# Kernel optimization log

Measured on AMD Instinct MI355X. Metric: run time of the kernel, lower is better.

## Reference

```python
import jax, jax.numpy as jnp
import numpy as np
from jax import lax

B, N, M = 4, 16384, 2048
C_IN = 64
RADII = (0.2, 0.4)
KS = (32, 64)
MLPS = ((64, 64, 128), (64, 96, 128))
EPS = 1e-5


def setup_inputs() -> dict:
    key = jax.random.key(0)
    ks = jax.random.split(key, 32)
    inp = {}
    inp["xyz"] = jax.random.uniform(ks[0], (B, 3, N), jnp.float32)
    inp["feature"] = jax.random.normal(ks[1], (B, C_IN, N), jnp.float32)
    ki = 2
    for s, chans in enumerate(MLPS):
        cin = C_IN + 3  # use_xyz concatenates relative xyz
        for l, cout in enumerate(chans):
            inp[f"w{s}{l}"] = jax.random.normal(ks[ki], (cout, cin), jnp.float32) * (1.0 / np.sqrt(cin)); ki += 1
            inp[f"g{s}{l}"] = jnp.ones((cout,), jnp.float32)
            inp[f"b{s}{l}"] = jnp.zeros((cout,), jnp.float32)
            cin = cout
    return inp


def _fps(points):
    """Farthest point sampling. points [N,3] -> [M] int32 indices (starts at 0)."""
    n = points.shape[0]
    def step(carry, _):
        dists, last = carry
        d = jnp.sum((points - points[last]) ** 2, axis=-1)
        dists = jnp.minimum(dists, d)
        nxt = jnp.argmax(dists).astype(jnp.int32)
        return (dists, nxt), nxt
    init = (jnp.full((n,), 1e10, jnp.float32), jnp.int32(0))
    _, rest = lax.scan(step, init, None, length=M - 1)
    return jnp.concatenate([jnp.zeros((1,), jnp.int32), rest])


def _ball_query(xyz, new_xyz, radius, k):
    """xyz [B,3,N], new_xyz [B,3,M] -> [B,M,k] int32. First-found semantics: empty
    slots are filled with the first valid index (pointnet2 ball_query behavior)."""
    xyz = lax.stop_gradient(xyz)
    new_xyz = lax.stop_gradient(new_xyz)
    n = xyz.shape[-1]
    sq_x = jnp.sum(xyz ** 2, axis=1)          # [B,N]
    sq_c = jnp.sum(new_xyz ** 2, axis=1)      # [B,M]
    d2 = sq_c[:, :, None] + sq_x[:, None, :] - 2.0 * jnp.einsum('bdm,bdn->bmn', new_xyz, xyz)
    scores = jnp.where(d2 < radius * radius, jnp.arange(n, dtype=jnp.int32), n)
    idx = -lax.top_k(-scores, k)[0]           # k smallest indices (in order)
    first = idx[..., :1]
    idx = jnp.where(idx >= n, first, idx)
    return jnp.where(idx >= n, 0, idx)


def _group(feat, idx):
    """feat [B,C,N], idx [B,M,K] -> [B,C,M,K]"""
    return jax.vmap(lambda f, i: f[:, i])(feat, idx)


def _forward(xyz, feature, params):
    idx = jax.vmap(_fps)(jnp.transpose(lax.stop_gradient(xyz), (0, 2, 1)))  # [B,M]
    new_xyz = jnp.take_along_axis(xyz, idx[:, None, :].astype(jnp.int32), axis=2)  # [B,3,M]
    feats = []
    for s in range(len(MLPS)):
        nidx = _ball_query(xyz, new_xyz, RADII[s], KS[s])        # [B,M,K]
        gxyz = _group(xyz, nidx) - new_xyz[..., None]            # [B,3,M,K]
        x = jnp.concatenate([gxyz, _group(feature, nidx)], axis=1)  # [B,3+C,M,K]
        for l in range(len(MLPS[s])):
            w = params[f"w{s}{l}"]; g = params[f"g{s}{l}"]; b = params[f"b{s}{l}"]
            x = jnp.einsum('oc,bcmk->bomk', w, x)                # 1x1 conv
            mu = jnp.mean(x, axis=(0, 2, 3), keepdims=True)      # train-mode BN
            var = jnp.mean((x - mu) ** 2, axis=(0, 2, 3), keepdims=True)
            x = (x - mu) * lax.rsqrt(var + EPS)
            x = x * g[None, :, None, None] + b[None, :, None, None]
            x = jax.nn.relu(x)
        feats.append(jnp.max(x, axis=3))                         # max over neighbors
    return new_xyz, jnp.concatenate(feats, axis=1)               # [B,3,M], [B,256,M]


def reference(xyz, feature, w00, g00, b00, w01, g01, b01, w02, g02, b02,
              w10, g10, b10, w11, g11, b11, w12, g12, b12):
    params = dict(w00=w00, g00=g00, b00=b00, w01=w01, g01=g01, b01=b01,
                  w02=w02, g02=g02, b02=b02, w10=w10, g10=g10, b10=b10,
                  w11=w11, g11=g11, b11=b11, w12=w12, g12=g12, b12=b12)
    return _forward(xyz, feature, params)
```

## Files before the change

kernel.cpp:

```cpp
#include <hip/hip_runtime.h>
#include <cstdint>

constexpr int B_ = 4, N_ = 16384, M_ = 2048;
constexpr int COLS0 = B_ * M_ * 32;
constexpr int COLS1 = B_ * M_ * 64;

constexpr size_t OFF_NEWXYZ = 0;
constexpr size_t OFF_NIDX0  = (size_t)B_ * 3 * M_ * 4;
constexpr size_t OFF_NIDX1  = OFF_NIDX0 + (size_t)COLS0 * 4;
constexpr size_t OFF_STATS  = OFF_NIDX1 + (size_t)COLS1 * 4;
constexpr size_t STATS_VALS = 64 * 2 * 128;
constexpr size_t OFF_COEF   = OFF_STATS + 6 * STATS_VALS * 8;
constexpr size_t OFF_Z      = OFF_COEF + 6 * 128 * 16;
constexpr int ZSTRIDE = 96 * 64;

__global__ __launch_bounds__(512, 2) void fps_kernel(const float* __restrict__ xyz,
                                                     float* __restrict__ newxyz,
                                                     float* __restrict__ outxyz) {
#pragma clang fp contract(off)
  int b = blockIdx.x, t = threadIdx.x;
  const float* xb = xyz + (size_t)b * 3 * N_;
  float px[32], py[32], pz[32], dd[32];
#pragma unroll
  for (int i = 0; i < 32; ++i) {
    int n = t + (i << 9);
    px[i] = xb[n]; py[i] = xb[N_ + n]; pz[i] = xb[2 * N_ + n];
    dd[i] = 1e10f;
    asm volatile("" : "+v"(px[i]), "+v"(py[i]), "+v"(pz[i]));
  }
  __shared__ float s_out[3 * M_];
  __shared__ unsigned long long s_red[8];
  __shared__ int s_w;
  float fx = xb[0], fy = xb[N_], fz = xb[2 * N_];
  if (t == 0) { s_out[0] = fx; s_out[M_] = fy; s_out[2 * M_] = fz; }
  int lane = t & 63, wid = t >> 6;
  for (int s = 1; s < M_; ++s) {
    float bv = -1.f; int bi = 0;
#pragma unroll
    for (int i = 0; i < 32; ++i) {
      float dx = px[i] - fx, dy = py[i] - fy, dz = pz[i] - fz;
      float d = (dx * dx + dy * dy) + dz * dz;
      float dm = dd[i];
      if (d < dm) dm = d;
      dd[i] = dm;
      if (dm > bv) { bv = dm; bi = t + (i << 9); }
    }
    unsigned long long key =
        ((unsigned long long)__float_as_uint(bv) << 32) | (unsigned)(0xFFFFFFFFu - (unsigned)bi);
#pragma unroll
    for (int off = 1; off < 64; off <<= 1) {
      unsigned long long o = __shfl_xor(key, off);
      if (o > key) key = o;
    }
    if (lane == 0) s_red[wid] = key;
    __syncthreads();
    if (wid == 0) {
      unsigned long long k2 = (lane < 8) ? s_red[lane] : 0ull;
#pragma unroll
      for (int off = 1; off < 8; off <<= 1) {
        unsigned long long o = __shfl_xor(k2, off);
        if (o > k2) k2 = o;
      }
      if (lane == 0) s_w = (int)(0xFFFFFFFFu - (unsigned)(k2 & 0xFFFFFFFFull));
    }
    __syncthreads();
    int w = s_w;
    fx = xb[w]; fy = xb[N_ + w]; fz = xb[2 * N_ + w];
    if (t == 0) { s_out[s] = fx; s_out[M_ + s] = fy; s_out[2 * M_ + s] = fz; }
  }
  __syncthreads();
  for (int e = t; e < 3 * M_; e += 512) {
    float v = s_out[e];
    newxyz[(size_t)b * 3 * M_ + e] = v;
    outxyz[(size_t)b * 3 * M_ + e] = v;
  }
}

template <int KNB>
__global__ __launch_bounds__(256) void bq_kernel(const float* __restrict__ xyz,
                                                 const float* __restrict__ newxyz,
                                                 int* __restrict__ nidx, float r2) {
#pragma clang fp contract(off)
  int t = threadIdx.x, lane = t & 63, wq = t >> 6;
  int q = blockIdx.x * 4 + wq;
  int b = q >> 11, m = q & 2047;
  const float* xb = xyz + (size_t)b * 3 * N_;
  float cx = newxyz[((size_t)b * 3 + 0) * M_ + m];
  float cy = newxyz[((size_t)b * 3 + 1) * M_ + m];
  float cz = newxyz[((size_t)b * 3 + 2) * M_ + m];
  float sqc = (cx * cx + cy * cy) + cz * cz;
  int found = 0, first = 0;
  for (int c = 0; c < N_ / 64; ++c) {
    int n = c * 64 + lane;
    float x = xb[n], y = xb[N_ + n], z = xb[2 * N_ + n];
    float sqx = (x * x + y * y) + z * z;
    float dot = fmaf(cz, z, fmaf(cy, y, cx * x));
    float d2 = (sqc + sqx) - 2.0f * dot;
    bool in = d2 < r2;
    unsigned long long mask = __ballot(in);
    if (mask) {
      if (found == 0) first = c * 64 + (__ffsll((long long)mask) - 1);
      int pos = found + __popcll(mask & ((1ull << lane) - 1ull));
      if (in && pos < KNB) nidx[(size_t)q * KNB + pos] = n;
      found += __popcll(mask);
      if (found >= KNB) break;
    }
  }
  if (found < KNB) {
    int fill = (found == 0) ? 0 : first;
    for (int s = found + lane; s < KNB; s += 64) nidx[(size_t)q * KNB + s] = fill;
  }
}

__device__ __forceinline__ void stat_accum(float acc, int o, int cout, double* stats,
                                           int part, int lane) {
  float v1 = acc, v2 = acc * acc;
#pragma unroll
  for (int off = 1; off < 64; off <<= 1) {
    v1 += __shfl_xor(v1, off);
    v2 += __shfl_xor(v2, off);
  }
  if (lane == 0) {
    atomicAdd(stats + ((size_t)part * 2 + 0) * cout + o, (double)v1);
    atomicAdd(stats + ((size_t)part * 2 + 1) * cout + o, (double)v2);
  }
}

template <int CIN, int G>
__device__ __forceinline__ void conv_sweep(const float* __restrict__ w, int o0,
                                           const float* sx, int lane, float* acc) {
  int o0u = __builtin_amdgcn_readfirstlane(o0);
  const float* wb = w + (size_t)o0u * CIN;
#pragma unroll
  for (int k = 0; k < G; ++k) acc[k] = 0.f;
#pragma unroll 8
  for (int c = 0; c < CIN; ++c) {
    float xv = sx[c * 64 + lane];
#pragma unroll
    for (int k = 0; k < G; ++k) acc[k] += wb[(size_t)(4 * k) * CIN + c] * xv;
  }
}

template <int CIN>
__device__ __forceinline__ void stage_bn(const float* __restrict__ zr,
                                         const float4* __restrict__ coefIn,
                                         float* sx, int t) {
  const float4* zr4 = (const float4*)zr;
  float4* sx4 = (float4*)sx;
  for (int e = t; e < CIN * 16; e += 256) {
    int c = e >> 4;
    float4 v = zr4[e];
    float4 cf = coefIn[c];
    float4 r;
    r.x = fmaxf(((v.x - cf.x) * cf.y) * cf.z + cf.w, 0.f);
    r.y = fmaxf(((v.y - cf.x) * cf.y) * cf.z + cf.w, 0.f);
    r.z = fmaxf(((v.z - cf.x) * cf.y) * cf.z + cf.w, 0.f);
    r.w = fmaxf(((v.w - cf.x) * cf.y) * cf.z + cf.w, 0.f);
    sx4[e] = r;
  }
}

template <int KNB>
__global__ __launch_bounds__(256) void convL0_kernel(
    const float* __restrict__ w0, const float* __restrict__ xyz,
    const float* __restrict__ feat, const int* __restrict__ nidx,
    const float* __restrict__ newxyz, float* __restrict__ Z, double* __restrict__ stats) {
  __shared__ float sx[67 * 64];
  __shared__ int snb[64];
  int rec = blockIdx.x, t = threadIdx.x, lane = t & 63, wid = t >> 6;
  if (t < 64) snb[t] = nidx[(size_t)rec * 64 + t];
  __syncthreads();
  for (int e = t; e < 67 * 64; e += 256) {
    int c = e >> 6, l = e & 63;
    int col = rec * 64 + l;
    int b = col / (M_ * KNB);
    int rem = col - b * (M_ * KNB);
    int m = rem / KNB;
    int n = snb[l];
    float v;
    if (c < 3) v = xyz[((size_t)b * 3 + c) * N_ + n] - newxyz[((size_t)b * 3 + c) * M_ + m];
    else       v = feat[((size_t)b * 64 + (c - 3)) * N_ + n];
    sx[e] = v;
  }
  __syncthreads();
  float* zr = Z + (size_t)rec * ZSTRIDE;
  int part = rec & 63;
  float acc[8];
#pragma unroll
  for (int g = 0; g < 2; ++g) {
    int o0 = wid + 32 * g;
    conv_sweep<67, 8>(w0, o0, sx, lane, acc);
#pragma unroll
    for (int k = 0; k < 8; ++k) {
      int o = o0 + 4 * k;
      zr[o * 64 + lane] = acc[k];
      stat_accum(acc[k], o, 64, stats, part, lane);
    }
  }
}

template <int CIN, int COUT>
__global__ __launch_bounds__(256) void convMid_kernel(
    const float* __restrict__ w, const float4* __restrict__ coefIn,
    float* __restrict__ Z, double* __restrict__ stats) {
  __shared__ float sx[CIN * 64];
  int rec = blockIdx.x, t = threadIdx.x, lane = t & 63, wid = t >> 6;
  float* zr = Z + (size_t)rec * ZSTRIDE;
  stage_bn<CIN>(zr, coefIn, sx, t);
  __syncthreads();
  int part = rec & 63;
  float acc[8];
#pragma unroll
  for (int g = 0; g < COUT / 32; ++g) {
    int o0 = wid + 32 * g;
    conv_sweep<CIN, 8>(w, o0, sx, lane, acc);
#pragma unroll
    for (int k = 0; k < 8; ++k) {
      int o = o0 + 4 * k;
      zr[o * 64 + lane] = acc[k];
      stat_accum(acc[k], o, COUT, stats, part, lane);
    }
  }
}

template <int CIN>
__global__ __launch_bounds__(256) void convLastStats_kernel(
    const float* __restrict__ w, const float4* __restrict__ coefIn,
    const float* __restrict__ Z, double* __restrict__ stats) {
  __shared__ float sx[CIN * 64];
  int rec = blockIdx.x, t = threadIdx.x, lane = t & 63, wid = t >> 6;
  const float* zr = Z + (size_t)rec * ZSTRIDE;
  stage_bn<CIN>(zr, coefIn, sx, t);
  __syncthreads();
  int part = rec & 63;
  float acc[8];
#pragma unroll
  for (int g = 0; g < 4; ++g) {
    int o0 = wid + 32 * g;
    conv_sweep<CIN, 8>(w, o0, sx, lane, acc);
#pragma unroll
    for (int k = 0; k < 8; ++k) stat_accum(acc[k], o0 + 4 * k, 128, stats, part, lane);
  }
}

template <int CIN, int KNB>
__global__ __launch_bounds__(256) void convLastPool_kernel(
    const float* __restrict__ w, const float4* __restrict__ coefIn,
    const float4* __restrict__ coefOut,
    const float* __restrict__ Z, float* __restrict__ outFeats, int chBase) {
  __shared__ float sx[CIN * 64];
  int rec = blockIdx.x, t = threadIdx.x, lane = t & 63, wid = t >> 6;
  const float* zr = Z + (size_t)rec * ZSTRIDE;
  stage_bn<CIN>(zr, coefIn, sx, t);
  __syncthreads();
  float acc[8];
#pragma unroll
  for (int g = 0; g < 4; ++g) {
    int o0 = wid + 32 * g;
    conv_sweep<CIN, 8>(w, o0, sx, lane, acc);
#pragma unroll
    for (int k = 0; k < 8; ++k) {
      int o = o0 + 4 * k;
      float4 cf = coefOut[o];
      float z = fmaxf(((acc[k] - cf.x) * cf.y) * cf.z + cf.w, 0.f);
      if (KNB == 64) {
#pragma unroll
        for (int off = 1; off < 64; off <<= 1) z = fmaxf(z, __shfl_xor(z, off));
        if (lane == 0) {
          int b = rec >> 11, m = rec & 2047;
          outFeats[((size_t)b * 256 + chBase + o) * M_ + m] = z;
        }
      } else {
#pragma unroll
        for (int off = 1; off < 32; off <<= 1) z = fmaxf(z, __shfl_xor(z, off));
        if ((lane & 31) == 0) {
          int grp = rec * 2 + (lane >> 5);
          int b = grp >> 11, m = grp & 2047;
          outFeats[((size_t)b * 256 + chBase + o) * M_ + m] = z;
        }
      }
    }
  }
}

__global__ void coef_kernel(const double* __restrict__ stats, const float* __restrict__ g,
                            const float* __restrict__ bb, float4* __restrict__ coef,
                            int cout, double invcnt) {
  int ch = threadIdx.x;
  if (ch >= cout) return;
  double s1 = 0.0, s2 = 0.0;
  for (int p = 0; p < 64; ++p) {
    s1 += stats[((size_t)p * 2 + 0) * cout + ch];
    s2 += stats[((size_t)p * 2 + 1) * cout + ch];
  }
  double mean = s1 * invcnt;
  double var = s2 * invcnt - mean * mean;
  double rstd = 1.0 / sqrt(var + 1e-5);
  coef[ch] = make_float4((float)mean, (float)rstd, g[ch], bb[ch]);
}

extern "C" void kernel_launch(void* const* d_in, const int* in_sizes, int n_in,
                              void* d_out, int out_size, void* d_ws, size_t ws_size,
                              hipStream_t stream) {
  const float* xyz  = (const float*)d_in[0];
  const float* feat = (const float*)d_in[1];
  const float* w00 = (const float*)d_in[2],  *g00 = (const float*)d_in[3],  *b00 = (const float*)d_in[4];
  const float* w01 = (const float*)d_in[5],  *g01 = (const float*)d_in[6],  *b01 = (const float*)d_in[7];
  const float* w02 = (const float*)d_in[8],  *g02 = (const float*)d_in[9],  *b02 = (const float*)d_in[10];
  const float* w10 = (const float*)d_in[11], *g10 = (const float*)d_in[12], *b10 = (const float*)d_in[13];
  const float* w11 = (const float*)d_in[14], *g11 = (const float*)d_in[15], *b11 = (const float*)d_in[16];
  const float* w12 = (const float*)d_in[17], *g12 = (const float*)d_in[18], *b12 = (const float*)d_in[19];

  char* ws = (char*)d_ws;
  float*  newxyz = (float*)(ws + OFF_NEWXYZ);
  int*    nidx0  = (int*)(ws + OFF_NIDX0);
  int*    nidx1  = (int*)(ws + OFF_NIDX1);
  double* stats  = (double*)(ws + OFF_STATS);
  float4* coef   = (float4*)(ws + OFF_COEF);
  float*  Z      = (float*)(ws + OFF_Z);
  float* outF = (float*)d_out;
  float* outFeats = outF + (size_t)B_ * 3 * M_;

  hipMemsetAsync(ws + OFF_STATS, 0, 6 * STATS_VALS * 8, stream);
  fps_kernel<<<B_, 512, 0, stream>>>(xyz, newxyz, outF);
  bq_kernel<32><<<(B_ * M_) / 4, 256, 0, stream>>>(xyz, newxyz, nidx0, (float)(0.2 * 0.2));
  bq_kernel<64><<<(B_ * M_) / 4, 256, 0, stream>>>(xyz, newxyz, nidx1, (float)(0.4 * 0.4));

  float4* c00 = coef + 0 * 128; float4* c01 = coef + 1 * 128; float4* c02 = coef + 2 * 128;
  float4* c10 = coef + 3 * 128; float4* c11 = coef + 4 * 128; float4* c12 = coef + 5 * 128;
  double* st0 = stats + 0 * STATS_VALS; double* st1 = stats + 1 * STATS_VALS;
  double* st2 = stats + 2 * STATS_VALS; double* st3 = stats + 3 * STATS_VALS;
  double* st4 = stats + 4 * STATS_VALS; double* st5 = stats + 5 * STATS_VALS;
  int gb0 = COLS0 / 64, gb1 = COLS1 / 64;

  convL0_kernel<32><<<gb0, 256, 0, stream>>>(w00, xyz, feat, nidx0, newxyz, Z, st0);
  coef_kernel<<<1, 128, 0, stream>>>(st0, g00, b00, c00, 64, 1.0 / COLS0);
  convMid_kernel<64, 64><<<gb0, 256, 0, stream>>>(w01, c00, Z, st1);
  coef_kernel<<<1, 128, 0, stream>>>(st1, g01, b01, c01, 64, 1.0 / COLS0);
  convLastStats_kernel<64><<<gb0, 256, 0, stream>>>(w02, c01, Z, st2);
  coef_kernel<<<1, 128, 0, stream>>>(st2, g02, b02, c02, 128, 1.0 / COLS0);
  convLastPool_kernel<64, 32><<<gb0, 256, 0, stream>>>(w02, c01, c02, Z, outFeats, 0);

  convL0_kernel<64><<<gb1, 256, 0, stream>>>(w10, xyz, feat, nidx1, newxyz, Z, st3);
  coef_kernel<<<1, 128, 0, stream>>>(st3, g10, b10, c10, 64, 1.0 / COLS1);
  convMid_kernel<64, 96><<<gb1, 256, 0, stream>>>(w11, c10, Z, st4);
  coef_kernel<<<1, 128, 0, stream>>>(st4, g11, b11, c11, 96, 1.0 / COLS1);
  convLastStats_kernel<96><<<gb1, 256, 0, stream>>>(w12, c11, Z, st5);
  coef_kernel<<<1, 128, 0, stream>>>(st5, g12, b12, c12, 128, 1.0 / COLS1);
  convLastPool_kernel<96, 64><<<gb1, 256, 0, stream>>>(w12, c11, c12, Z, outFeats, 128);
}
```

Baseline: 5.056 ms.

## Replace second last-layer conv pass with per-group min/max and tiny finalize kernel

The last layer of each scale was computed twice, once to gather batch-norm statistics and once to apply BN, ReLU and the max-pool. Because BN is an affine map per channel, the pooled result can be recovered from the per-group max and min of the raw conv output. The stats pass now also writes these, and a small elementwise kernel applies the coefficients once they are known. This removes a full conv sweep per scale at the cost of extra shuffle reductions and four workspace buffers.

New measurement: 4.894 ms, median of 2. -3.2%, faster.

```diff
diff --git a/kernel.cpp b/kernel.cpp
--- a/kernel.cpp
+++ b/kernel.cpp
@@ -11,7 +11,9 @@
 constexpr size_t OFF_STATS  = OFF_NIDX1 + (size_t)COLS1 * 4;
 constexpr size_t STATS_VALS = 64 * 2 * 128;
 constexpr size_t OFF_COEF   = OFF_STATS + 6 * STATS_VALS * 8;
-constexpr size_t OFF_Z      = OFF_COEF + 6 * 128 * 16;
+constexpr size_t OFF_MNMX   = OFF_COEF + 6 * 128 * 16;
+constexpr size_t MNMX_ONE   = (size_t)B_ * M_ * 128 * 4;
+constexpr size_t OFF_Z      = OFF_MNMX + 4 * MNMX_ONE;
 constexpr int ZSTRIDE = 96 * 64;
 
 __global__ __launch_bounds__(512, 2) void fps_kernel(const float* __restrict__ xyz,
@@ -223,10 +225,11 @@
   }
 }
 
-template <int CIN>
-__global__ __launch_bounds__(256) void convLastStats_kernel(
+template <int CIN, int KNB>
+__global__ __launch_bounds__(256) void convLast_kernel(
     const float* __restrict__ w, const float4* __restrict__ coefIn,
-    const float* __restrict__ Z, double* __restrict__ stats) {
+    const float* __restrict__ Z, double* __restrict__ stats,
+    float* __restrict__ mx, float* __restrict__ mn) {
   __shared__ float sx[CIN * 64];
   int rec = blockIdx.x, t = threadIdx.x, lane = t & 63, wid = t >> 6;
   const float* zr = Z + (size_t)rec * ZSTRIDE;
@@ -239,48 +242,49 @@
     int o0 = wid + 32 * g;
     conv_sweep<CIN, 8>(w, o0, sx, lane, acc);
 #pragma unroll
-    for (int k = 0; k < 8; ++k) stat_accum(acc[k], o0 + 4 * k, 128, stats, part, lane);
-  }
-}
-
-template <int CIN, int KNB>
-__global__ __launch_bounds__(256) void convLastPool_kernel(
-    const float* __restrict__ w, const float4* __restrict__ coefIn,
-    const float4* __restrict__ coefOut,
-    const float* __restrict__ Z, float* __restrict__ outFeats, int chBase) {
-  __shared__ float sx[CIN * 64];
-  int rec = blockIdx.x, t = threadIdx.x, lane = t & 63, wid = t >> 6;
-  const float* zr = Z + (size_t)rec * ZSTRIDE;
-  stage_bn<CIN>(zr, coefIn, sx, t);
-  __syncthreads();
-  float acc[8];
-#pragma unroll
-  for (int g = 0; g < 4; ++g) {
-    int o0 = wid + 32 * g;
-    conv_sweep<CIN, 8>(w, o0, sx, lane, acc);
-#pragma unroll
     for (int k = 0; k < 8; ++k) {
       int o = o0 + 4 * k;
-      float4 cf = coefOut[o];
-      float z = fmaxf(((acc[k] - cf.x) * cf.y) * cf.z + cf.w, 0.f);
+      stat_accum(acc[k], o, 128, stats, part, lane);
+      float vM = acc[k], vN = acc[k];
       if (KNB == 64) {
 #pragma unroll
-        for (int off = 1; off < 64; off <<= 1) z = fmaxf(z, __shfl_xor(z, off));
+        for (int off = 1; off < 64; off <<= 1) {
+          vM = fmaxf(vM, __shfl_xor(vM, off));
+          vN = fminf(vN, __shfl_xor(vN, off));
+        }
         if (lane == 0) {
-          int b = rec >> 11, m = rec & 2047;
-          outFeats[((size_t)b * 256 + chBase + o) * M_ + m] = z;
+          mx[(size_t)o * (B_ * M_) + rec] = vM;
+          mn[(size_t)o * (B_ * M_) + rec] = vN;
         }
       } else {
 #pragma unroll
-        for (int off = 1; off < 32; off <<= 1) z = fmaxf(z, __shfl_xor(z, off));
+        for (int off = 1; off < 32; off <<= 1) {
+          vM = fmaxf(vM, __shfl_xor(vM, off));
+          vN = fminf(vN, __shfl_xor(vN, off));
+        }
         if ((lane & 31) == 0) {
           int grp = rec * 2 + (lane >> 5);
-          int b = grp >> 11, m = grp & 2047;
-          outFeats[((size_t)b * 256 + chBase + o) * M_ + m] = z;
+          mx[(size_t)o * (B_ * M_) + grp] = vM;
+          mn[(size_t)o * (B_ * M_) + grp] = vN;
         }
       }
     }
   }
+}
+
+__global__ __launch_bounds__(256) void pool_fin_kernel(
+    const float* __restrict__ mx, const float* __restrict__ mn,
+    const float4* __restrict__ coefOut, float* __restrict__ outFeats, int chBase) {
+  int idx = blockIdx.x * 256 + threadIdx.x;
+  int o = idx >> 13;
+  int gm = idx & 8191;
+  float4 cf = coefOut[o];
+  float vM = mx[idx], vN = mn[idx];
+  float rM = ((vM - cf.x) * cf.y) * cf.z + cf.w;
+  float rN = ((vN - cf.x) * cf.y) * cf.z + cf.w;
+  float z = fmaxf(fmaxf(rM, rN), 0.f);
+  int b = gm >> 11, m = gm & 2047;
+  outFeats[((size_t)b * 256 + chBase + o) * M_ + m] = z;
 }
 
 __global__ void coef_kernel(const double* __restrict__ stats, const float* __restrict__ g,
@@ -317,6 +321,10 @@
   int*    nidx1  = (int*)(ws + OFF_NIDX1);
   double* stats  = (double*)(ws + OFF_STATS);
   float4* coef   = (float4*)(ws + OFF_COEF);
+  float*  mx0    = (float*)(ws + OFF_MNMX + 0 * MNMX_ONE);
+  float*  mn0    = (float*)(ws + OFF_MNMX + 1 * MNMX_ONE);
+  float*  mx1    = (float*)(ws + OFF_MNMX + 2 * MNMX_ONE);
+  float*  mn1    = (float*)(ws + OFF_MNMX + 3 * MNMX_ONE);
   float*  Z      = (float*)(ws + OFF_Z);
   float* outF = (float*)d_out;
   float* outFeats = outF + (size_t)B_ * 3 * M_;
@@ -332,20 +340,21 @@
   double* st2 = stats + 2 * STATS_VALS; double* st3 = stats + 3 * STATS_VALS;
   double* st4 = stats + 4 * STATS_VALS; double* st5 = stats + 5 * STATS_VALS;
   int gb0 = COLS0 / 64, gb1 = COLS1 / 64;
+  int gfin = (128 * B_ * M_) / 256;
 
   convL0_kernel<32><<<gb0, 256, 0, stream>>>(w00, xyz, feat, nidx0, newxyz, Z, st0);
   coef_kernel<<<1, 128, 0, stream>>>(st0, g00, b00, c00, 64, 1.0 / COLS0);
   convMid_kernel<64, 64><<<gb0, 256, 0, stream>>>(w01, c00, Z, st1);
   coef_kernel<<<1, 128, 0, stream>>>(st1, g01, b01, c01, 64, 1.0 / COLS0);
-  convLastStats_kernel<64><<<gb0, 256, 0, stream>>>(w02, c01, Z, st2);
+  convLast_kernel<64, 32><<<gb0, 256, 0, stream>>>(w02, c01, Z, st2, mx0, mn0);
   coef_kernel<<<1, 128, 0, stream>>>(st2, g02, b02, c02, 128, 1.0 / COLS0);
-  convLastPool_kernel<64, 32><<<gb0, 256, 0, stream>>>(w02, c01, c02, Z, outFeats, 0);
+  pool_fin_kernel<<<gfin, 256, 0, stream>>>(mx0, mn0, c02, outFeats, 0);
 
   convL0_kernel<64><<<gb1, 256, 0, stream>>>(w10, xyz, feat, nidx1, newxyz, Z, st3);
   coef_kernel<<<1, 128, 0, stream>>>(st3, g10, b10, c10, 64, 1.0 / COLS1);
   convMid_kernel<64, 96><<<gb1, 256, 0, stream>>>(w11, c10, Z, st4);
   coef_kernel<<<1, 128, 0, stream>>>(st4, g11, b11, c11, 96, 1.0 / COLS1);
-  convLastStats_kernel<96><<<gb1, 256, 0, stream>>>(w12, c11, Z, st5);
+  convLast_kernel<96, 64><<<gb1, 256, 0, stream>>>(w12, c11, Z, st5, mx1, mn1);
   coef_kernel<<<1, 128, 0, stream>>>(st5, g12, b12, c12, 128, 1.0 / COLS1);
-  convLastPool_kernel<96, 64><<<gb1, 256, 0, stream>>>(w12, c11, c12, Z, outFeats, 128);
-}
+  pool_fin_kernel<<<gfin, 256, 0, stream>>>(mx1, mn1, c12, outFeats, 128);
+}
```
